# Performance work log

Measured on AMD Instinct MI355X. Metric: run time of the kernel, lower is better.

The kernel has to match this reference:

```python
import jax, jax.numpy as jnp
import numpy as np

H = 128
T = 120
F_IN = 180
BN_EPS = 1e-5
LEAKY_SLOPE = 0.01


def _lstm_layer(x, wih, whh, bih, bhh):
    """Single LSTM layer. x: (B,T,D); wih:(4H,D), whh:(4H,H). PyTorch gate order i,f,g,o."""
    B = x.shape[0]
    # Precompute input projections for all timesteps: (B,T,4H)
    x_proj = jnp.einsum('btd,gd->btg', x, wih) + bih + bhh
    x_proj = jnp.transpose(x_proj, (1, 0, 2))  # (T,B,4H) for scan over time
    h0 = jnp.zeros((B, H), dtype=x.dtype)
    c0 = jnp.zeros((B, H), dtype=x.dtype)

    def step(carry, xt):
        h, c = carry
        gates = xt + h @ whh.T  # (B,4H)
        i, f, g, o = jnp.split(gates, 4, axis=-1)
        i = jax.nn.sigmoid(i)
        f = jax.nn.sigmoid(f)
        g = jnp.tanh(g)
        o = jax.nn.sigmoid(o)
        c = f * c + i * g
        h = o * jnp.tanh(c)
        return (h, c), h

    (_, _), hs = jax.lax.scan(step, (h0, c0), x_proj)  # hs: (T,B,H)
    return jnp.transpose(hs, (1, 0, 2))  # (B,T,H)


def setup_inputs() -> dict:
    key = jax.random.key(0)
    ks = jax.random.split(key, 16)
    B = 2048
    s = 0.1  # keep activations in a stable range
    inp = {
        'x': jax.random.normal(ks[0], (B, F_IN, T), jnp.float32),
        'fc_w': jax.random.normal(ks[1], (H, F_IN), jnp.float32) * s,
        'fc_b': jax.random.normal(ks[2], (H,), jnp.float32) * s,
        'bn_g': jax.random.uniform(ks[3], (H,), jnp.float32, 0.5, 1.5),
        'bn_b': jax.random.normal(ks[4], (H,), jnp.float32) * s,
        'bn_mean': jax.random.normal(ks[5], (H,), jnp.float32) * s,
        'bn_var': jax.random.uniform(ks[6], (H,), jnp.float32, 0.5, 1.5),
        'wih0': jax.random.normal(ks[7], (4 * H, H), jnp.float32) * s,
        'whh0': jax.random.normal(ks[8], (4 * H, H), jnp.float32) * s,
        'bih0': jax.random.normal(ks[9], (4 * H,), jnp.float32) * s,
        'bhh0': jax.random.normal(ks[10], (4 * H,), jnp.float32) * s,
        'wih1': jax.random.normal(ks[11], (4 * H, H), jnp.float32) * s,
        'whh1': jax.random.normal(ks[12], (4 * H, H), jnp.float32) * s,
        'bih1': jax.random.normal(ks[13], (4 * H,), jnp.float32) * s,
        'bhh1': jax.random.normal(ks[14], (4 * H,), jnp.float32) * s,
    }
    return inp


def reference(x, fc_w, fc_b, bn_g, bn_b, bn_mean, bn_var,
              wih0, whh0, bih0, bhh0, wih1, whh1, bih1, bhh1):
    # x.reshape(-1,180,120).permute(0,2,1) -> (B,120,180)
    h = jnp.transpose(x.reshape(-1, F_IN, T), (0, 2, 1)).reshape(-1, F_IN)
    # Linear + BatchNorm1d (eval mode) + LeakyReLU
    h = h @ fc_w.T + fc_b
    h = (h - bn_mean) * jax.lax.rsqrt(bn_var + BN_EPS) * bn_g + bn_b
    h = jnp.where(h >= 0, h, LEAKY_SLOPE * h)
    h = h.reshape(-1, T, H)
    # 2-layer LSTM, take last timestep
    h = _lstm_layer(h, wih0, whh0, bih0, bhh0)
    h = _lstm_layer(h, wih1, whh1, bih1, bhh1)
    return h[:, -1, :]
```

## Files before the change

kernel.cpp:

```cpp
#include <hip/hip_runtime.h>

#define T_STEPS 120
#define NF_IN   180
#define H_DIM   128
#define G_DIM   512
#define F_PAD   200
#define K_FC    192

typedef __attribute__((ext_vector_type(8))) short short8;
typedef __attribute__((ext_vector_type(4))) float f32x4;

__device__ __forceinline__ f32x4 mfma16(short8 a, short8 b, f32x4 c) {
    return __builtin_amdgcn_mfma_f32_16x16x32_bf16(a, b, c, 0, 0, 0);
}

__device__ __forceinline__ short f2bf(float x) {
    union { float f; unsigned u; } v; v.f = x;
    unsigned r = v.u + 0x7fffu + ((v.u >> 16) & 1u);
    return (short)(r >> 16);
}

__device__ __forceinline__ float sigm(float x) {
    return __builtin_amdgcn_rcpf(1.f + __expf(-x));
}
__device__ __forceinline__ float tanh_f(float x) {
    return 1.f - 2.f * __builtin_amdgcn_rcpf(1.f + __expf(2.f * x));
}

__global__ void prep_kernel(
    const float* __restrict__ fc_w, const float* __restrict__ fc_b,
    const float* __restrict__ bn_g, const float* __restrict__ bn_b,
    const float* __restrict__ bn_mean, const float* __restrict__ bn_var,
    const float* __restrict__ wih0, const float* __restrict__ whh0,
    const float* __restrict__ bih0, const float* __restrict__ bhh0,
    const float* __restrict__ wih1, const float* __restrict__ whh1,
    const float* __restrict__ bih1, const float* __restrict__ bhh1,
    short* __restrict__ fcw_o, float* __restrict__ fcb_o,
    float* __restrict__ bias0_o, float* __restrict__ bias1_o,
    short* __restrict__ wih0_o, short* __restrict__ whh0_o,
    short* __restrict__ wih1_o, short* __restrict__ whh1_o)
{
    int tid = blockIdx.x * blockDim.x + threadIdx.x;
    int stride = gridDim.x * blockDim.x;
    for (int i = tid; i < H_DIM * K_FC; i += stride) {
        int h = i / K_FC, f = i % K_FC;
        float s = bn_g[h] * rsqrtf(bn_var[h] + 1e-5f);
        float v = (f < NF_IN) ? fc_w[h * NF_IN + f] * s : 0.f;
        fcw_o[i] = f2bf(v);
    }
    for (int i = tid; i < H_DIM; i += stride) {
        float s = bn_g[i] * rsqrtf(bn_var[i] + 1e-5f);
        fcb_o[i] = (fc_b[i] - bn_mean[i]) * s + bn_b[i];
    }
    for (int i = tid; i < G_DIM; i += stride) {
        bias0_o[i] = bih0[i] + bhh0[i];
        bias1_o[i] = bih1[i] + bhh1[i];
    }
    for (int i = tid; i < G_DIM * H_DIM; i += stride) {
        wih0_o[i] = f2bf(wih0[i]); whh0_o[i] = f2bf(whh0[i]);
        wih1_o[i] = f2bf(wih1[i]); whh1_o[i] = f2bf(whh1[i]);
    }
}

__global__ __launch_bounds__(256) void fc_kernel(
    const float* __restrict__ x, const short* __restrict__ fcw,
    const float* __restrict__ fcb, short* __restrict__ h0)
{
    __shared__ short xs[128 * F_PAD];
    const int b = blockIdx.x;
    const int tid = threadIdx.x;

    for (int i = tid; i < 128 * F_PAD / 2; i += 256) ((unsigned*)xs)[i] = 0u;
    __syncthreads();

    const float* xb = x + (size_t)b * (NF_IN * T_STEPS);
    for (int i = tid; i < (NF_IN * T_STEPS / 4); i += 256) {
        int f = i / 30, t4 = (i % 30) * 4;
        float4 v = *(const float4*)(xb + f * T_STEPS + t4);
        xs[(t4 + 0) * F_PAD + f] = f2bf(v.x);
        xs[(t4 + 1) * F_PAD + f] = f2bf(v.y);
        xs[(t4 + 2) * F_PAD + f] = f2bf(v.z);
        xs[(t4 + 3) * F_PAD + f] = f2bf(v.w);
    }
    __syncthreads();

    const int wave = tid >> 6, lane = tid & 63;
    const int m16 = lane & 15, q = lane >> 4;

    short8 af[2][6];
#pragma unroll
    for (int mi = 0; mi < 2; ++mi) {
        int t = (wave * 2 + mi) * 16 + m16;
#pragma unroll
        for (int kc = 0; kc < 6; ++kc)
            af[mi][kc] = *(const short8*)(xs + t * F_PAD + kc * 32 + q * 8);
    }

    float fcb_v[8];
#pragma unroll
    for (int nt = 0; nt < 8; ++nt) fcb_v[nt] = fcb[nt * 16 + m16];

    f32x4 acc[2][8];
#pragma unroll
    for (int mi = 0; mi < 2; ++mi)
#pragma unroll
        for (int nt = 0; nt < 8; ++nt) acc[mi][nt] = (f32x4){0.f, 0.f, 0.f, 0.f};

#pragma unroll
    for (int nt = 0; nt < 8; ++nt) {
        short8 bf[6];
#pragma unroll
        for (int kc = 0; kc < 6; ++kc)
            bf[kc] = *(const short8*)(fcw + (nt * 16 + m16) * K_FC + kc * 32 + q * 8);
#pragma unroll
        for (int mi = 0; mi < 2; ++mi)
#pragma unroll
            for (int kc = 0; kc < 6; ++kc)
                acc[mi][nt] = mfma16(af[mi][kc], bf[kc], acc[mi][nt]);
    }
    __syncthreads();

    short* outs = xs;
#pragma unroll
    for (int mi = 0; mi < 2; ++mi)
#pragma unroll
        for (int nt = 0; nt < 8; ++nt)
#pragma unroll
            for (int r = 0; r < 4; ++r) {
                int t = (wave * 2 + mi) * 16 + q * 4 + r;
                int h = nt * 16 + m16;
                float v = acc[mi][nt][r] + fcb_v[nt];
                v = (v >= 0.f) ? v : 0.01f * v;
                outs[t * H_DIM + h] = f2bf(v);
            }
    __syncthreads();

    unsigned* dst = (unsigned*)h0 + (size_t)b * (T_STEPS * H_DIM / 2);
    const unsigned* srcs = (const unsigned*)outs;
    for (int i = tid; i < T_STEPS * H_DIM / 2; i += 256) dst[i] = srcs[i];
}

__global__ __launch_bounds__(512, 2) void lstm_kernel(
    const short* h_in,
    const short* __restrict__ wih,
    const short* __restrict__ whh,
    const float* __restrict__ bias,
    short* h_out,
    float* __restrict__ fout)
{
    __shared__ short h_lds[16 * H_DIM];
    __shared__ float gates_lds[8 * G_DIM];
    __shared__ float xp_lds[2][8 * G_DIM];

    const int tid = threadIdx.x;
    const int wave = tid >> 6, lane = tid & 63;
    const int m16 = lane & 15, q = lane >> 4;
    const int b0 = blockIdx.x * 8;
    const bool is_prod = wave >= 4;
    const int slice = (wave & 3) * 128;

    for (int i = tid; i < 16 * H_DIM / 2; i += 512) ((unsigned*)h_lds)[i] = 0u;

    const short* W = is_prod ? wih : whh;
    short8 wf[8][4];
#pragma unroll
    for (int nt = 0; nt < 8; ++nt)
#pragma unroll
        for (int kc = 0; kc < 4; ++kc)
            wf[nt][kc] = *(const short8*)(W + (slice + nt * 16 + m16) * H_DIM + kc * 32 + q * 8);

    float bias_v[8];
#pragma unroll
    for (int nt = 0; nt < 8; ++nt) bias_v[nt] = bias[slice + nt * 16 + m16];

    const int urow = wave & 7;
    const int ud = (lane) * 2;
    float c0 = 0.f, c1 = 0.f;

    auto producer = [&](int t1, int buf) {
        short8 af[4];
        int m = (m16 < 8) ? m16 : 0;
        const short* src = h_in + ((size_t)(b0 + m) * T_STEPS + t1) * H_DIM + q * 8;
#pragma unroll
        for (int kc = 0; kc < 4; ++kc) af[kc] = *(const short8*)(src + kc * 32);
#pragma unroll
        for (int nt = 0; nt < 8; ++nt) {
            f32x4 acc = (f32x4){bias_v[nt], bias_v[nt], bias_v[nt], bias_v[nt]};
#pragma unroll
            for (int kc = 0; kc < 4; ++kc) acc = mfma16(af[kc], wf[nt][kc], acc);
            if (q < 2) {
#pragma unroll
                for (int r = 0; r < 4; ++r)
                    xp_lds[buf][(q * 4 + r) * G_DIM + slice + nt * 16 + m16] = acc[r];
            }
        }
    };

    if (is_prod) producer(0, 0);
    __syncthreads();

    for (int t = 0; t < T_STEPS; ++t) {
        if (!is_prod) {
            short8 af[4];
#pragma unroll
            for (int kc = 0; kc < 4; ++kc)
                af[kc] = *(const short8*)(h_lds + m16 * H_DIM + kc * 32 + q * 8);
#pragma unroll
            for (int nt = 0; nt < 8; ++nt) {
                f32x4 acc = (f32x4){0.f, 0.f, 0.f, 0.f};
#pragma unroll
                for (int kc = 0; kc < 4; ++kc) acc = mfma16(af[kc], wf[nt][kc], acc);
                if (q < 2) {
#pragma unroll
                    for (int r = 0; r < 4; ++r)
                        gates_lds[(q * 4 + r) * G_DIM + slice + nt * 16 + m16] = acc[r];
                }
            }
        } else if (t + 1 < T_STEPS) {
            producer(t + 1, (t + 1) & 1);
        }
        __syncthreads();

        {
            const float* gb = gates_lds;
            const float* xb = xp_lds[t & 1];
            int base = urow * G_DIM + ud;
            float2 ri = *(const float2*)(gb + base);
            float2 rf = *(const float2*)(gb + base + 128);
            float2 rg = *(const float2*)(gb + base + 256);
            float2 ro = *(const float2*)(gb + base + 384);
            float2 xi = *(const float2*)(xb + base);
            float2 xf = *(const float2*)(xb + base + 128);
            float2 xg = *(const float2*)(xb + base + 256);
            float2 xo = *(const float2*)(xb + base + 384);
            float i0 = sigm(ri.x + xi.x), i1 = sigm(ri.y + xi.y);
            float ff0 = sigm(rf.x + xf.x), ff1 = sigm(rf.y + xf.y);
            float g0 = tanh_f(rg.x + xg.x), g1 = tanh_f(rg.y + xg.y);
            float o0 = sigm(ro.x + xo.x), o1 = sigm(ro.y + xo.y);
            c0 = ff0 * c0 + i0 * g0;
            c1 = ff1 * c1 + i1 * g1;
            float hh0 = o0 * tanh_f(c0);
            float hh1 = o1 * tanh_f(c1);
            unsigned packed = (unsigned)(unsigned short)f2bf(hh0) |
                              ((unsigned)(unsigned short)f2bf(hh1) << 16);
            *(unsigned*)(h_lds + urow * H_DIM + ud) = packed;
            if (h_out)
                *(unsigned*)(h_out + ((size_t)(b0 + urow) * T_STEPS + t) * H_DIM + ud) = packed;
            if (fout && t == T_STEPS - 1) {
                float2 hv; hv.x = hh0; hv.y = hh1;
                *(float2*)(fout + (size_t)(b0 + urow) * H_DIM + ud) = hv;
            }
        }
        __syncthreads();
    }
}

static constexpr size_t OFF_FCW  = 0;
static constexpr size_t OFF_FCB  = 49152;
static constexpr size_t OFF_B0   = 49664;
static constexpr size_t OFF_B1   = 51712;
static constexpr size_t OFF_WIH0 = 53760;
static constexpr size_t OFF_WHH0 = 184832;
static constexpr size_t OFF_WIH1 = 315904;
static constexpr size_t OFF_WHH1 = 446976;
static constexpr size_t OFF_BUFA = 578048;

extern "C" void kernel_launch(void* const* d_in, const int* in_sizes, int n_in,
                              void* d_out, int out_size, void* d_ws, size_t ws_size,
                              hipStream_t stream) {
    const float* x       = (const float*)d_in[0];
    const float* fc_w    = (const float*)d_in[1];
    const float* fc_b    = (const float*)d_in[2];
    const float* bn_g    = (const float*)d_in[3];
    const float* bn_b    = (const float*)d_in[4];
    const float* bn_mean = (const float*)d_in[5];
    const float* bn_var  = (const float*)d_in[6];
    const float* wih0    = (const float*)d_in[7];
    const float* whh0    = (const float*)d_in[8];
    const float* bih0    = (const float*)d_in[9];
    const float* bhh0    = (const float*)d_in[10];
    const float* wih1    = (const float*)d_in[11];
    const float* whh1    = (const float*)d_in[12];
    const float* bih1    = (const float*)d_in[13];
    const float* bhh1    = (const float*)d_in[14];

    const int B = in_sizes[0] / (NF_IN * T_STEPS);

    char* ws = (char*)d_ws;
    short* fcw   = (short*)(ws + OFF_FCW);
    float* fcb   = (float*)(ws + OFF_FCB);
    float* bias0 = (float*)(ws + OFF_B0);
    float* bias1 = (float*)(ws + OFF_B1);
    short* wih0b = (short*)(ws + OFF_WIH0);
    short* whh0b = (short*)(ws + OFF_WHH0);
    short* wih1b = (short*)(ws + OFF_WIH1);
    short* whh1b = (short*)(ws + OFF_WHH1);
    short* bufA  = (short*)(ws + OFF_BUFA);

    prep_kernel<<<256, 256, 0, stream>>>(
        fc_w, fc_b, bn_g, bn_b, bn_mean, bn_var,
        wih0, whh0, bih0, bhh0, wih1, whh1, bih1, bhh1,
        fcw, fcb, bias0, bias1, wih0b, whh0b, wih1b, whh1b);

    fc_kernel<<<B, 256, 0, stream>>>(x, fcw, fcb, bufA);

    lstm_kernel<<<B / 8, 512, 0, stream>>>(bufA, wih0b, whh0b, bias0, bufA, nullptr);
    lstm_kernel<<<B / 8, 512, 0, stream>>>(bufA, wih1b, whh1b, bias1, nullptr, (float*)d_out);
}
```

Before: 697.1 us.

## Fuse LSTM gate math into consumer waves and double-buffer h to halve barriers

The LSTM step no longer routes recurrent gate results through LDS for a separate elementwise pass. Each consumer wave now owns all four gates for a 32-column slice and applies the cell update in registers. The hidden state is double-buffered, so each step needs one barrier instead of two, and the h_out write is deferred one step and spread across all waves. The fc kernel now gathers x straight from global memory into MFMA fragments instead of staging a transpose in LDS, which may give uncoalesced strided loads. Only four waves now do the gate math, so the elementwise work per lane grows.

```diff
diff --git a/kernel.cpp b/kernel.cpp
--- a/kernel.cpp
+++ b/kernel.cpp
@@ -4,8 +4,9 @@
 #define NF_IN   180
 #define H_DIM   128
 #define G_DIM   512
-#define F_PAD   200
 #define K_FC    192
+#define HP      136
+#define XP_TILE 4096
 
 typedef __attribute__((ext_vector_type(8))) short short8;
 typedef __attribute__((ext_vector_type(4))) float f32x4;
@@ -64,26 +65,11 @@
 
 __global__ __launch_bounds__(256) void fc_kernel(
     const float* __restrict__ x, const short* __restrict__ fcw,
-    const float* __restrict__ fcb, short* __restrict__ h0)
+    const float* __restrict__ fcb, short* __restrict__ xfc)
 {
-    __shared__ short xs[128 * F_PAD];
+    __shared__ short outs[120 * 132];
     const int b = blockIdx.x;
     const int tid = threadIdx.x;
-
-    for (int i = tid; i < 128 * F_PAD / 2; i += 256) ((unsigned*)xs)[i] = 0u;
-    __syncthreads();
-
-    const float* xb = x + (size_t)b * (NF_IN * T_STEPS);
-    for (int i = tid; i < (NF_IN * T_STEPS / 4); i += 256) {
-        int f = i / 30, t4 = (i % 30) * 4;
-        float4 v = *(const float4*)(xb + f * T_STEPS + t4);
-        xs[(t4 + 0) * F_PAD + f] = f2bf(v.x);
-        xs[(t4 + 1) * F_PAD + f] = f2bf(v.y);
-        xs[(t4 + 2) * F_PAD + f] = f2bf(v.z);
-        xs[(t4 + 3) * F_PAD + f] = f2bf(v.w);
-    }
-    __syncthreads();
-
     const int wave = tid >> 6, lane = tid & 63;
     const int m16 = lane & 15, q = lane >> 4;
 
@@ -91,9 +77,19 @@
 #pragma unroll
     for (int mi = 0; mi < 2; ++mi) {
         int t = (wave * 2 + mi) * 16 + m16;
-#pragma unroll
-        for (int kc = 0; kc < 6; ++kc)
-            af[mi][kc] = *(const short8*)(xs + t * F_PAD + kc * 32 + q * 8);
+        if (t > 119) t = 119;
+        const float* xb = x + (size_t)b * (NF_IN * T_STEPS) + (size_t)q * 8 * T_STEPS + t;
+#pragma unroll
+        for (int kc = 0; kc < 6; ++kc) {
+            union { short s[8]; short8 v; } u;
+#pragma unroll
+            for (int j = 0; j < 8; ++j) {
+                int f = kc * 32 + q * 8 + j;
+                float val = (f < NF_IN) ? xb[(kc * 32 + j) * T_STEPS] : 0.f;
+                u.s[j] = f2bf(val);
+            }
+            af[mi][kc] = u.v;
+        }
     }
 
     float fcb_v[8];
@@ -118,9 +114,7 @@
             for (int kc = 0; kc < 6; ++kc)
                 acc[mi][nt] = mfma16(af[mi][kc], bf[kc], acc[mi][nt]);
     }
-    __syncthreads();
-
-    short* outs = xs;
+
 #pragma unroll
     for (int mi = 0; mi < 2; ++mi)
 #pragma unroll
@@ -131,13 +125,16 @@
                 int h = nt * 16 + m16;
                 float v = acc[mi][nt][r] + fcb_v[nt];
                 v = (v >= 0.f) ? v : 0.01f * v;
-                outs[t * H_DIM + h] = f2bf(v);
+                if (t < 120) outs[t * 132 + h] = f2bf(v);
             }
     __syncthreads();
 
-    unsigned* dst = (unsigned*)h0 + (size_t)b * (T_STEPS * H_DIM / 2);
+    unsigned* dst = (unsigned*)xfc + (size_t)b * (T_STEPS * H_DIM / 2);
     const unsigned* srcs = (const unsigned*)outs;
-    for (int i = tid; i < T_STEPS * H_DIM / 2; i += 256) dst[i] = srcs[i];
+    for (int i = tid; i < T_STEPS * H_DIM / 2; i += 256) {
+        int t = i >> 6, c2 = i & 63;
+        dst[i] = srcs[t * 66 + c2];
+    }
 }
 
 __global__ __launch_bounds__(512, 2) void lstm_kernel(
@@ -148,110 +145,115 @@
     short* h_out,
     float* __restrict__ fout)
 {
-    __shared__ short h_lds[16 * H_DIM];
-    __shared__ float gates_lds[8 * G_DIM];
-    __shared__ float xp_lds[2][8 * G_DIM];
+    __shared__ short h_lds[2 * 8 * HP];
+    __shared__ float xp_lds[2 * XP_TILE];
 
     const int tid = threadIdx.x;
     const int wave = tid >> 6, lane = tid & 63;
-    const int m16 = lane & 15, q = lane >> 4;
+    const int q = lane >> 4, m16 = lane & 15, m8 = m16 & 7;
+    const int qv = q & 1;
     const int b0 = blockIdx.x * 8;
-    const bool is_prod = wave >= 4;
-    const int slice = (wave & 3) * 128;
-
-    for (int i = tid; i < 16 * H_DIM / 2; i += 512) ((unsigned*)h_lds)[i] = 0u;
-
-    const short* W = is_prod ? wih : whh;
-    short8 wf[8][4];
-#pragma unroll
-    for (int nt = 0; nt < 8; ++nt)
-#pragma unroll
-        for (int kc = 0; kc < 4; ++kc)
-            wf[nt][kc] = *(const short8*)(W + (slice + nt * 16 + m16) * H_DIM + kc * 32 + q * 8);
-
-    float bias_v[8];
-#pragma unroll
-    for (int nt = 0; nt < 8; ++nt) bias_v[nt] = bias[slice + nt * 16 + m16];
-
-    const int urow = wave & 7;
-    const int ud = (lane) * 2;
-    float c0 = 0.f, c1 = 0.f;
-
-    auto producer = [&](int t1, int buf) {
-        short8 af[4];
-        int m = (m16 < 8) ? m16 : 0;
-        const short* src = h_in + ((size_t)(b0 + m) * T_STEPS + t1) * H_DIM + q * 8;
-#pragma unroll
-        for (int kc = 0; kc < 4; ++kc) af[kc] = *(const short8*)(src + kc * 32);
-#pragma unroll
-        for (int nt = 0; nt < 8; ++nt) {
-            f32x4 acc = (f32x4){bias_v[nt], bias_v[nt], bias_v[nt], bias_v[nt]};
-#pragma unroll
-            for (int kc = 0; kc < 4; ++kc) acc = mfma16(af[kc], wf[nt][kc], acc);
-            if (q < 2) {
-#pragma unroll
-                for (int r = 0; r < 4; ++r)
-                    xp_lds[buf][(q * 4 + r) * G_DIM + slice + nt * 16 + m16] = acc[r];
+    const bool cons = wave < 4;
+    const int d = wave & 3;
+
+    for (int i = tid; i < 8 * HP; i += 512) ((unsigned*)h_lds)[i] = 0u;
+
+    const short* W = cons ? whh : wih;
+    short8 wf[4][2][4];
+    float bias_v[4][2];
+#pragma unroll
+    for (int g = 0; g < 4; ++g)
+#pragma unroll
+        for (int j = 0; j < 2; ++j) {
+            int n = g * 128 + d * 32 + j * 16 + m16;
+            bias_v[g][j] = bias[n];
+#pragma unroll
+            for (int kc = 0; kc < 4; ++kc)
+                wf[g][j][kc] = *(const short8*)(W + n * H_DIM + kc * 32 + q * 8);
+        }
+
+    float c[2][4];
+#pragma unroll
+    for (int j = 0; j < 2; ++j)
+#pragma unroll
+        for (int r = 0; r < 4; ++r) c[j][r] = 0.f;
+
+    auto prod = [&](int t) {
+        const short* src = h_in + ((size_t)(b0 + m8) * T_STEPS + t) * H_DIM + q * 8;
+        short8 ax[4];
+#pragma unroll
+        for (int kc = 0; kc < 4; ++kc) ax[kc] = *(const short8*)(src + kc * 32);
+        float* xpb = xp_lds + (t & 1) * XP_TILE;
+#pragma unroll
+        for (int g = 0; g < 4; ++g)
+#pragma unroll
+            for (int j = 0; j < 2; ++j) {
+                float bv = bias_v[g][j];
+                f32x4 acc = (f32x4){bv, bv, bv, bv};
+#pragma unroll
+                for (int kc = 0; kc < 4; ++kc) acc = mfma16(ax[kc], wf[g][j][kc], acc);
+                if (q < 2)
+                    *(f32x4*)(xpb + ((d * 8 + g * 2 + j) * 16 + m16) * 8 + q * 4) = acc;
             }
-        }
     };
 
-    if (is_prod) producer(0, 0);
+    if (!cons) prod(0);
     __syncthreads();
 
-    for (int t = 0; t < T_STEPS; ++t) {
-        if (!is_prod) {
-            short8 af[4];
-#pragma unroll
-            for (int kc = 0; kc < 4; ++kc)
-                af[kc] = *(const short8*)(h_lds + m16 * H_DIM + kc * 32 + q * 8);
-#pragma unroll
-            for (int nt = 0; nt < 8; ++nt) {
-                f32x4 acc = (f32x4){0.f, 0.f, 0.f, 0.f};
-#pragma unroll
-                for (int kc = 0; kc < 4; ++kc) acc = mfma16(af[kc], wf[nt][kc], acc);
-                if (q < 2) {
-#pragma unroll
-                    for (int r = 0; r < 4; ++r)
-                        gates_lds[(q * 4 + r) * G_DIM + slice + nt * 16 + m16] = acc[r];
+    for (int s = 0; s < T_STEPS; ++s) {
+        if (cons) {
+            const short* hb = h_lds + ((s + 1) & 1) * (8 * HP) + m8 * HP + q * 8;
+            short8 ar[4];
+#pragma unroll
+            for (int kc = 0; kc < 4; ++kc) ar[kc] = *(const short8*)(hb + kc * 32);
+            f32x4 racc[4][2];
+#pragma unroll
+            for (int g = 0; g < 4; ++g)
+#pragma unroll
+                for (int j = 0; j < 2; ++j) {
+                    f32x4 acc = (f32x4){0.f, 0.f, 0.f, 0.f};
+#pragma unroll
+                    for (int kc = 0; kc < 4; ++kc) acc = mfma16(ar[kc], wf[g][j][kc], acc);
+                    racc[g][j] = acc;
+                }
+            const float* xpb = xp_lds + (s & 1) * XP_TILE;
+            short* hw = h_lds + (s & 1) * (8 * HP);
+#pragma unroll
+            for (int j = 0; j < 2; ++j) {
+                f32x4 xv[4];
+#pragma unroll
+                for (int g = 0; g < 4; ++g)
+                    xv[g] = *(const f32x4*)(xpb + ((d * 8 + g * 2 + j) * 16 + m16) * 8 + qv * 4);
+#pragma unroll
+                for (int r = 0; r < 4; ++r) {
+                    float iv = sigm(racc[0][j][r] + xv[0][r]);
+                    float fv = sigm(racc[1][j][r] + xv[1][r]);
+                    float gv = tanh_f(racc[2][j][r] + xv[2][r]);
+                    float ov = sigm(racc[3][j][r] + xv[3][r]);
+                    float cc = fv * c[j][r] + iv * gv;
+                    c[j][r] = cc;
+                    float hv = ov * tanh_f(cc);
+                    if (q < 2) {
+                        hw[(q * 4 + r) * HP + d * 32 + j * 16 + m16] = f2bf(hv);
+                        if (fout != nullptr && s == T_STEPS - 1)
+                            fout[(size_t)(b0 + q * 4 + r) * H_DIM + d * 32 + j * 16 + m16] = hv;
+                    }
                 }
             }
-        } else if (t + 1 < T_STEPS) {
-            producer(t + 1, (t + 1) & 1);
+        } else {
+            if (s + 1 < T_STEPS) prod(s + 1);
+        }
+        if (h_out != nullptr && s >= 1) {
+            int row = tid >> 6, c2 = tid & 63;
+            unsigned v = ((const unsigned*)h_lds)[((s + 1) & 1) * (4 * HP) + row * (HP / 2) + c2];
+            ((unsigned*)h_out)[((size_t)(b0 + row) * T_STEPS + (s - 1)) * (H_DIM / 2) + c2] = v;
         }
         __syncthreads();
-
-        {
-            const float* gb = gates_lds;
-            const float* xb = xp_lds[t & 1];
-            int base = urow * G_DIM + ud;
-            float2 ri = *(const float2*)(gb + base);
-            float2 rf = *(const float2*)(gb + base + 128);
-            float2 rg = *(const float2*)(gb + base + 256);
-            float2 ro = *(const float2*)(gb + base + 384);
-            float2 xi = *(const float2*)(xb + base);
-            float2 xf = *(const float2*)(xb + base + 128);
-            float2 xg = *(const float2*)(xb + base + 256);
-            float2 xo = *(const float2*)(xb + base + 384);
-            float i0 = sigm(ri.x + xi.x), i1 = sigm(ri.y + xi.y);
-            float ff0 = sigm(rf.x + xf.x), ff1 = sigm(rf.y + xf.y);
-            float g0 = tanh_f(rg.x + xg.x), g1 = tanh_f(rg.y + xg.y);
-            float o0 = sigm(ro.x + xo.x), o1 = sigm(ro.y + xo.y);
-            c0 = ff0 * c0 + i0 * g0;
-            c1 = ff1 * c1 + i1 * g1;
-            float hh0 = o0 * tanh_f(c0);
-            float hh1 = o1 * tanh_f(c1);
-            unsigned packed = (unsigned)(unsigned short)f2bf(hh0) |
-                              ((unsigned)(unsigned short)f2bf(hh1) << 16);
-            *(unsigned*)(h_lds + urow * H_DIM + ud) = packed;
-            if (h_out)
-                *(unsigned*)(h_out + ((size_t)(b0 + urow) * T_STEPS + t) * H_DIM + ud) = packed;
-            if (fout && t == T_STEPS - 1) {
-                float2 hv; hv.x = hh0; hv.y = hh1;
-                *(float2*)(fout + (size_t)(b0 + urow) * H_DIM + ud) = hv;
-            }
-        }
-        __syncthreads();
+    }
+    if (h_out != nullptr) {
+        int row = tid >> 6, c2 = tid & 63;
+        unsigned v = ((const unsigned*)h_lds)[1 * (4 * HP) + row * (HP / 2) + c2];
+        ((unsigned*)h_out)[((size_t)(b0 + row) * T_STEPS + (T_STEPS - 1)) * (H_DIM / 2) + c2] = v;
     }
 }
 
```

After: 654.6 us. -6.1%, faster.
